# Kernel tuning notes

Hardware: AMD Instinct MI355X
Metric: run time of the kernel (lower is better)

Reference implementation:

```python
import jax, jax.numpy as jnp
import numpy as np

N_STATE = 1024
N_HEAD = 16
HEAD_DIM = N_STATE // N_HEAD


def setup_inputs() -> dict:
    key = jax.random.key(0)
    ks = jax.random.split(key, 8)
    s = 0.02
    return {
        "x": jax.random.normal(ks[0], (4, 1500, N_STATE), dtype=jnp.float32),
        "Wq": jax.random.normal(ks[1], (N_STATE, N_STATE), dtype=jnp.float32) * s,
        "bq": jnp.zeros((N_STATE,), dtype=jnp.float32),
        "Wk": jax.random.normal(ks[2], (N_STATE, N_STATE), dtype=jnp.float32) * s,
        "Wv": jax.random.normal(ks[3], (N_STATE, N_STATE), dtype=jnp.float32) * s,
        "bv": jnp.zeros((N_STATE,), dtype=jnp.float32),
        "Wo": jax.random.normal(ks[4], (N_STATE, N_STATE), dtype=jnp.float32) * s,
        "bo": jnp.zeros((N_STATE,), dtype=jnp.float32),
    }


def reference(x, Wq, bq, Wk, Wv, bv, Wo, bo):
    B, S, _ = x.shape
    scale = HEAD_DIM ** (-0.5)
    # projections (torch Linear: y = x @ W.T + b)
    q = x @ Wq.T + bq
    k = x @ Wk.T
    v = x @ Wv.T + bv
    # [B, H, S, D]
    q = q.reshape(B, S, N_HEAD, HEAD_DIM).transpose(0, 2, 1, 3)
    k = k.reshape(B, S, N_HEAD, HEAD_DIM).transpose(0, 2, 1, 3)
    v = v.reshape(B, S, N_HEAD, HEAD_DIM).transpose(0, 2, 1, 3)
    # scores scaled AFTER the matmul, as in the original (qk * qk_scale)
    qk = jnp.einsum("bhqd,bhkd->bhqk", q, k) * scale
    w = jax.nn.softmax(qk, axis=-1)
    wv = jnp.einsum("bhqk,bhkd->bhqd", w, v)
    wv = wv.transpose(0, 2, 1, 3).reshape(B, S, N_STATE)
    return wv @ Wo.T + bo
```

## Files before the change

kernel.cpp:

```cpp
#include <hip/hip_runtime.h>
#include <stdint.h>

#define S_LEN  1500
#define S_PAD  1536
#define BATCH  4
#define NSTATE 1024
#define NHEAD  16
#define HDIM   64
#define MROWS  6000
#define C1 0.180336879f

typedef __attribute__((ext_vector_type(8)))  short short8;
typedef __attribute__((ext_vector_type(4)))  float floatx4;
typedef __attribute__((ext_vector_type(16))) float floatx16;

__device__ __forceinline__ unsigned short f2bf(float f) {
  union { float f; unsigned int u; } v; v.f = f;
  unsigned int r = v.u + 0x7fffu + ((v.u >> 16) & 1u);
  return (unsigned short)(r >> 16);
}

__device__ __forceinline__ void gld_lds16(const void* g, void* l) {
  __builtin_amdgcn_global_load_lds(
      (const __attribute__((address_space(1))) void*)g,
      (__attribute__((address_space(3))) void*)l, 16, 0, 0);
}

__global__ __launch_bounds__(256) void cvt_all(
    const float* __restrict__ x,  const float* __restrict__ Wq,
    const float* __restrict__ Wk, const float* __restrict__ Wv,
    const float* __restrict__ Wo, unsigned short* __restrict__ dst,
    unsigned short* __restrict__ vt)
{
  const size_t NX   = (size_t)MROWS * NSTATE;
  const size_t NTOT = NX + 4u * 1024u * 1024u;
  size_t e = ((size_t)blockIdx.x * 256 + threadIdx.x) * 4;
  if (e >= NTOT) {
    size_t p = (e - NTOT) >> 2;
    int row = (int)(p / 9);
    int off = (int)(p % 9) * 4;
    uint2 z; z.x = 0u; z.y = 0u;
    *(uint2*)&vt[(size_t)row * S_PAD + 1500 + off] = z;
    return;
  }
  const float* src; size_t off;
  if (e < NX) { src = x; off = e; }
  else {
    size_t t = e - NX;
    int wsel = (int)(t >> 20);
    off = t & ((1u << 20) - 1);
    src = (wsel == 0) ? Wq : (wsel == 1) ? Wk : (wsel == 2) ? Wv : Wo;
  }
  float4 v = *(const float4*)(src + off);
  uint2 o;
  o.x = (unsigned int)f2bf(v.x) | ((unsigned int)f2bf(v.y) << 16);
  o.y = (unsigned int)f2bf(v.z) | ((unsigned int)f2bf(v.w) << 16);
  *(uint2*)(dst + e) = o;
}

__device__ __forceinline__ void gemm128_32(
    const unsigned short* __restrict__ X,
    const unsigned short* __restrict__ W,
    const float* __restrict__ bias,
    void* __restrict__ Yv,
    int m0, int n0, float oscale, int outmode)
{
  __shared__ unsigned short As[2][128 * 32];
  __shared__ unsigned short Bs[2][128 * 32];

  const int tid  = threadIdx.x;
  const int lane = tid & 63;
  const int wid  = tid >> 6;
  const int wm   = (wid & 1) * 64;
  const int wn   = (wid >> 1) * 64;
  const int l31  = lane & 31;
  const int lhi  = lane >> 5;
  const int fr   = (l31 >> 1) & 3;

  floatx16 acc[2][2];
#pragma unroll
  for (int i = 0; i < 2; ++i)
#pragma unroll
    for (int j = 0; j < 2; ++j)
      acc[i][j] = (floatx16)(0.f);

  const int srow = tid >> 2;
  const int logc = (lane & 3) ^ ((srow >> 1) & 3);

  const char* xrp[2];
  const char* wrp[2];
#pragma unroll
  for (int r = 0; r < 2; ++r) {
    int arow = m0 + r * 64 + srow;
    if (arow > MROWS - 1) arow = MROWS - 1;
    xrp[r] = (const char*)X + (size_t)arow * NSTATE * 2 + logc * 16;
    int brow = n0 + r * 64 + srow;
    wrp[r] = (const char*)W + (size_t)brow * NSTATE * 2 + logc * 16;
  }

  for (int k0 = 0; k0 < NSTATE; k0 += 64) {
    __syncthreads();
#pragma unroll
    for (int h = 0; h < 2; ++h) {
      int kb = (k0 + h * 32) * 2;
#pragma unroll
      for (int r = 0; r < 2; ++r) {
        gld_lds16(xrp[r] + kb, (char*)As[h] + r * 4096 + wid * 1024);
        gld_lds16(wrp[r] + kb, (char*)Bs[h] + r * 4096 + wid * 1024);
      }
    }
    __syncthreads();

#pragma unroll
    for (int h = 0; h < 2; ++h) {
      short8 af[2][2], bf[2][2];
#pragma unroll
      for (int mt = 0; mt < 2; ++mt)
#pragma unroll
        for (int kc = 0; kc < 2; ++kc) {
          int row  = wm + mt * 32 + l31;
          int phys = (kc * 2 + lhi) ^ fr;
          af[mt][kc] = *(const short8*)(As[h] + row * 32 + phys * 8);
        }
#pragma unroll
      for (int nt = 0; nt < 2; ++nt)
#pragma unroll
        for (int kc = 0; kc < 2; ++kc) {
          int row  = wn + nt * 32 + l31;
          int phys = (kc * 2 + lhi) ^ fr;
          bf[nt][kc] = *(const short8*)(Bs[h] + row * 32 + phys * 8);
        }
#pragma unroll
      for (int mt = 0; mt < 2; ++mt)
#pragma unroll
        for (int nt = 0; nt < 2; ++nt)
#pragma unroll
          for (int kc = 0; kc < 2; ++kc)
            acc[mt][nt] = __builtin_amdgcn_mfma_f32_32x32x16_bf16(
                af[mt][kc], bf[nt][kc], acc[mt][nt], 0, 0, 0);
    }
  }

  if (outmode == 2) {
    unsigned short* vt = (unsigned short*)Yv;
#pragma unroll
    for (int nt = 0; nt < 2; ++nt) {
      int ng = n0 + wn + nt * 32 + l31;
      float bias_v = bias[ng];
      int d  = ng & 63;
      int hh = ng >> 6;
#pragma unroll
      for (int mt = 0; mt < 2; ++mt)
#pragma unroll
        for (int rq = 0; rq < 4; ++rq) {
          int mgq = m0 + wm + mt * 32 + 8 * rq + 4 * lhi;
          if (mgq < MROWS) {
            int bb = mgq / 1500;
            int s0 = mgq - 1500 * bb;
            float v0 = acc[mt][nt][rq * 4 + 0] + bias_v;
            float v1 = acc[mt][nt][rq * 4 + 1] + bias_v;
            float v2 = acc[mt][nt][rq * 4 + 2] + bias_v;
            float v3 = acc[mt][nt][rq * 4 + 3] + bias_v;
            uint2 pk2;
            pk2.x = (unsigned int)f2bf(v0) | ((unsigned int)f2bf(v1) << 16);
            pk2.y = (unsigned int)f2bf(v2) | ((unsigned int)f2bf(v3) << 16);
            *(uint2*)&vt[(((size_t)bb * NHEAD + hh) * HDIM + d) * S_PAD + s0] = pk2;
          }
        }
    }
  } else {
#pragma unroll
    for (int nt = 0; nt < 2; ++nt) {
      int ng = n0 + wn + nt * 32 + l31;
      float bias_v = bias ? bias[ng] : 0.f;
#pragma unroll
      for (int mt = 0; mt < 2; ++mt)
#pragma unroll
        for (int r = 0; r < 16; ++r) {
          int mg = m0 + wm + mt * 32 + (r & 3) + 8 * (r >> 2) + 4 * lhi;
          if (mg < MROWS) {
            float val = (acc[mt][nt][r] + bias_v) * oscale;
            if (outmode == 1) ((float*)Yv)[(size_t)mg * NSTATE + ng] = val;
            else ((unsigned short*)Yv)[(size_t)mg * NSTATE + ng] = f2bf(val);
          }
        }
    }
  }
}

__global__ __launch_bounds__(256) void proj_qkv(
    const unsigned short* __restrict__ X,
    const unsigned short* __restrict__ Wq, const unsigned short* __restrict__ Wk,
    const unsigned short* __restrict__ Wv,
    const float* __restrict__ bq, const float* __restrict__ bv,
    unsigned short* __restrict__ q, unsigned short* __restrict__ k,
    unsigned short* __restrict__ vt)
{
  const int id  = blockIdx.x;
  const int sid = (id & 7) * 141 + (id >> 3);
  const int z   = sid / 376;
  const int rem = sid - z * 376;
  const int m0  = (rem >> 3) * 128;
  const int n0  = (rem & 7) * 128;

  if (z == 0)      gemm128_32(X, Wq, bq, q,  m0, n0, C1,  0);
  else if (z == 1) gemm128_32(X, Wk, (const float*)nullptr, k, m0, n0, 1.0f, 0);
  else             gemm128_32(X, Wv, bv, vt, m0, n0, 1.0f, 2);
}

__global__ __launch_bounds__(256) void proj_o(
    const unsigned short* __restrict__ X, const unsigned short* __restrict__ W,
    const float* __restrict__ bias, float* __restrict__ Y)
{
  const int id  = blockIdx.x;
  const int sid = (id & 7) * 47 + (id >> 3);
  gemm128_32(X, W, bias, Y, (sid >> 3) * 128, (sid & 7) * 128, 1.0f, 1);
}

#define NHALF 24

__global__ __launch_bounds__(256, 4) void attn32t(
    const unsigned short* __restrict__ Q, const unsigned short* __restrict__ K,
    const unsigned short* __restrict__ VT, unsigned short* __restrict__ O)
{
  __shared__ unsigned short SMEM[16384];
  unsigned short* Os = SMEM;

  const int tid  = threadIdx.x;
  const int lane = tid & 63;
  const int w    = tid >> 6;
  const int l31  = lane & 31;
  const int lhi  = lane >> 5;

  const int id  = blockIdx.x;
  const int sid = (id & 7) * 96 + (id >> 3);
  const int qt  = sid % 12;
  const int hb  = sid / 12;
  const int h   = hb & 15;
  const int b   = hb >> 4;

  const size_t base  = ((size_t)b * S_LEN) * NSTATE + h * HDIM;
  const size_t vbase = (((size_t)b * NHEAD + h) * HDIM) * S_PAD;

  const int srow8 = lane >> 3;
  const int sc3   = lane & 7;
  const int swc   = sc3 ^ srow8;

  const char* kq0 = (const char*)K +
      (base + (size_t)(w * 16 + srow8) * NSTATE + (size_t)swc * 8) * 2;
  const char* kq1 = kq0 + (size_t)8 * NSTATE * 2;
  const char* vq0 = (const char*)VT +
      (vbase + (size_t)(w * 16 + srow8) * S_PAD + (size_t)swc * 8) * 2;
  const char* vq1 = vq0 + (size_t)8 * S_PAD * 2;

  short8 qf[4];
  {
    int qrow = qt * 128 + w * 32 + l31;
    if (qrow > S_LEN - 1) qrow = S_LEN - 1;
    const unsigned short* qp = Q + base + (size_t)qrow * NSTATE;
#pragma unroll
    for (int c = 0; c < 4; ++c)
      qf[c] = *(const short8*)(qp + c * 16 + lhi * 8);
  }

  short8 ones8;
#pragma unroll
  for (int i = 0; i < 8; ++i) ones8[i] = (short)0x3F80;

  floatx16 oacc[2];
  oacc[0] = (floatx16)(0.f);
  oacc[1] = (floatx16)(0.f);
  floatx16 lacc = (floatx16)(0.f);

  auto stageN = [&](int u, int bi) {
    char* kb = (char*)SMEM + bi * 8192;
    char* vb = (char*)SMEM + 16384 + bi * 8192;
    size_t ko = (size_t)u * (64 * NSTATE * 2);
    size_t vo = (size_t)u * (64 * 2);
    gld_lds16(kq0 + ko, kb + (w * 2 + 0) * 1024);
    gld_lds16(kq1 + ko, kb + (w * 2 + 1) * 1024);
    gld_lds16(vq0 + vo, vb + (w * 2 + 0) * 1024);
    gld_lds16(vq1 + vo, vb + (w * 2 + 1) * 1024);
  };
  auto stageC = [&](int bi) {
    char* kb = (char*)SMEM + bi * 8192;
    char* vb = (char*)SMEM + 16384 + bi * 8192;
#pragma unroll
    for (int qq = 0; qq < 2; ++qq) {
      int s = 1472 + w * 16 + qq * 8 + srow8;
      if (s > S_LEN - 1) s = S_LEN - 1;
      gld_lds16((const char*)K + (base + (size_t)s * NSTATE + (size_t)swc * 8) * 2,
                kb + (w * 2 + qq) * 1024);
    }
    size_t vo = (size_t)23 * (64 * 2);
    gld_lds16(vq0 + vo, vb + (w * 2 + 0) * 1024);
    gld_lds16(vq1 + vo, vb + (w * 2 + 1) * 1024);
  };

  stageN(0, 0);
  __syncthreads();

  for (int u = 0; u < NHALF; ++u) {
    const int cur = u & 1;
    if (u < NHALF - 2)       stageN(u + 1, cur ^ 1);
    else if (u == NHALF - 2) stageC(cur ^ 1);

    const unsigned short* Ks  = SMEM + cur * 4096;
    const unsigned short* Vts = SMEM + 8192 + cur * 4096;

#pragma unroll
    for (int kvt = 0; kvt < 2; ++kvt) {
      int row = kvt * 32 + l31;
      floatx16 sacc = (floatx16)(0.f);
      __builtin_amdgcn_s_setprio(1);
#pragma unroll
      for (int c = 0; c < 4; ++c) {
        int phys = (c * 2 + lhi) ^ (row & 7);
        short8 ak = *(const short8*)(Ks + row * 64 + phys * 8);
        sacc = __builtin_amdgcn_mfma_f32_32x32x16_bf16(ak, qf[c], sacc, 0, 0, 0);
      }
      __builtin_amdgcn_s_setprio(0);

      if (u == NHALF - 1) {
        if (kvt == 1) {
#pragma unroll
          for (int r = 0; r < 16; ++r) sacc[r] = -3.0e38f;
        } else {
#pragma unroll
          for (int r = 12; r < 16; ++r) sacc[r] = lhi ? -3.0e38f : sacc[r];
        }
      }

      unsigned int pk[8];
#pragma unroll
      for (int i = 0; i < 8; ++i) {
        float plo = exp2f(sacc[2 * i]);
        float phi = exp2f(sacc[2 * i + 1]);
        unsigned int rr;
        asm("v_cvt_pk_bf16_f32 %0, %1, %2" : "=v"(rr) : "v"(plo), "v"(phi));
        pk[i] = rr;
      }

      unsigned int a0 = pk[0], a1 = pk[1], b0 = pk[2], b1 = pk[3];
      asm("v_permlane32_swap_b32 %0, %1" : "+v"(a0), "+v"(b0));
      asm("v_permlane32_swap_b32 %0, %1" : "+v"(a1), "+v"(b1));
      unsigned int c0 = pk[4], c1 = pk[5], d0 = pk[6], d1 = pk[7];
      asm("v_permlane32_swap_b32 %0, %1" : "+v"(c0), "+v"(d0));
      asm("v_permlane32_swap_b32 %0, %1" : "+v"(c1), "+v"(d1));
      int4 f0i, f1i;
      f0i.x = a0; f0i.y = a1; f0i.z = b0; f0i.w = b1;
      f1i.x = c0; f1i.y = c1; f1i.z = d0; f1i.w = d1;
      short8 f0 = *(short8*)&f0i;
      short8 f1 = *(short8*)&f1i;

      __builtin_amdgcn_s_setprio(1);
      lacc = __builtin_amdgcn_mfma_f32_32x32x16_bf16(ones8, f0, lacc, 0, 0, 0);
      lacc = __builtin_amdgcn_mfma_f32_32x32x16_bf16(ones8, f1, lacc, 0, 0, 0);

#pragma unroll
      for (int dt = 0; dt < 2; ++dt) {
        int d = dt * 32 + l31;
        int p0 = ((kvt * 4 + 0) + lhi) ^ (d & 7);
        int p1 = ((kvt * 4 + 2) + lhi) ^ (d & 7);
        short8 av0 = *(const short8*)(Vts + d * 64 + p0 * 8);
        short8 av1 = *(const short8*)(Vts + d * 64 + p1 * 8);
        oacc[dt] = __builtin_amdgcn_mfma_f32_32x32x16_bf16(av0, f0, oacc[dt], 0, 0, 0);
        oacc[dt] = __builtin_amdgcn_mfma_f32_32x32x16_bf16(av1, f1, oacc[dt], 0, 0, 0);
      }
      __builtin_amdgcn_s_setprio(0);
    }

    __syncthreads();
  }

  float inv = 1.f / lacc[0];

  __syncthreads();
#pragma unroll
  for (int dt = 0; dt < 2; ++dt)
#pragma unroll
    for (int g = 0; g < 4; ++g) {
      int d0 = dt * 32 + g * 8 + lhi * 4;
      float v0 = oacc[dt][4 * g + 0] * inv;
      float v1 = oacc[dt][4 * g + 1] * inv;
      float v2 = oacc[dt][4 * g + 2] * inv;
      float v3 = oacc[dt][4 * g + 3] * inv;
      uint2 pk2;
      pk2.x = (unsigned int)f2bf(v0) | ((unsigned int)f2bf(v1) << 16);
      pk2.y = (unsigned int)f2bf(v2) | ((unsigned int)f2bf(v3) << 16);
      *(uint2*)&Os[(w * 32 + l31) * 72 + d0] = pk2;
    }
  __syncthreads();
#pragma unroll
  for (int pass = 0; pass < 4; ++pass) {
    int e = pass * 256 + tid;
    int row = e >> 3, ch = e & 7;
    int s = qt * 128 + row;
    if (s < S_LEN)
      *(uint4*)&O[base + (size_t)s * NSTATE + ch * 8] = *(const uint4*)&Os[row * 72 + ch * 8];
  }
}

extern "C" void kernel_launch(void* const* d_in, const int* in_sizes, int n_in,
                              void* d_out, int out_size, void* d_ws, size_t ws_size,
                              hipStream_t stream) {
  const float* x  = (const float*)d_in[0];
  const float* Wq = (const float*)d_in[1];
  const float* bq = (const float*)d_in[2];
  const float* Wk = (const float*)d_in[3];
  const float* Wv = (const float*)d_in[4];
  const float* bv = (const float*)d_in[5];
  const float* Wo = (const float*)d_in[6];
  const float* bo = (const float*)d_in[7];
  float* out = (float*)d_out;

  const size_t NX  = (size_t)MROWS * NSTATE;
  const size_t NW  = (size_t)NSTATE * NSTATE;

  unsigned short* xb  = (unsigned short*)d_ws;
  unsigned short* Wqb = xb  + NX;
  unsigned short* Wkb = Wqb + NW;
  unsigned short* Wvb = Wkb + NW;
  unsigned short* Wob = Wvb + NW;
  unsigned short* q   = Wob + NW;
  unsigned short* k   = q + NX;
  unsigned short* vt  = k + NX;
  unsigned short* wv  = xb;

  const size_t n4_total = (NX + 4 * NW) / 4;
  const int main_blocks = (int)(n4_total / 256);
  const int pad_blocks  = (BATCH * NHEAD * HDIM * 9) / 256;
  cvt_all<<<dim3(main_blocks + pad_blocks), dim3(256), 0, stream>>>(
      x, Wq, Wk, Wv, Wo, xb, vt);
  proj_qkv<<<dim3(1128), dim3(256), 0, stream>>>(xb, Wqb, Wkb, Wvb, bq, bv, q, k, vt);
  attn32t<<<dim3(768), dim3(256), 0, stream>>>(q, k, vt, wv);
  proj_o<<<dim3(376), dim3(256), 0, stream>>>(wv, Wob, bo, out);
}
```

Before: 240.3 us.

## Double-buffer GEMM K-loop so global-to-LDS loads overlap MFMA compute

The projection GEMM K-loop now uses the two LDS halves as a ping-pong buffer: it prefetches the next 32-wide K slice while computing on the current one, going from one barrier pair per 64-K step to a single barrier per 32-K step. It also raises wave priority around the MFMA block. The intent is to hide global load latency behind matrix math. The trade-off is more loop iterations with less work each, and a reliance on barrier ordering of the async LDS loads for correctness.

```diff
diff --git a/kernel.cpp b/kernel.cpp
--- a/kernel.cpp
+++ b/kernel.cpp
@@ -98,47 +98,50 @@
     wrp[r] = (const char*)W + (size_t)brow * NSTATE * 2 + logc * 16;
   }
 
-  for (int k0 = 0; k0 < NSTATE; k0 += 64) {
+  auto stage = [&](int t, int bi) {
+    const int kb = t * 64;
+    gld_lds16(xrp[0] + kb, (char*)As[bi] + 0 * 4096 + wid * 1024);
+    gld_lds16(xrp[1] + kb, (char*)As[bi] + 1 * 4096 + wid * 1024);
+    gld_lds16(wrp[0] + kb, (char*)Bs[bi] + 0 * 4096 + wid * 1024);
+    gld_lds16(wrp[1] + kb, (char*)Bs[bi] + 1 * 4096 + wid * 1024);
+  };
+
+  stage(0, 0);
+  __syncthreads();
+
+  for (int t = 0; t < 32; ++t) {
+    const int cur = t & 1;
+    if (t < 31) stage(t + 1, cur ^ 1);
+
+    short8 af[2][2], bf[2][2];
+#pragma unroll
+    for (int mt = 0; mt < 2; ++mt)
+#pragma unroll
+      for (int kc = 0; kc < 2; ++kc) {
+        int row  = wm + mt * 32 + l31;
+        int phys = (kc * 2 + lhi) ^ fr;
+        af[mt][kc] = *(const short8*)(As[cur] + row * 32 + phys * 8);
+      }
+#pragma unroll
+    for (int nt = 0; nt < 2; ++nt)
+#pragma unroll
+      for (int kc = 0; kc < 2; ++kc) {
+        int row  = wn + nt * 32 + l31;
+        int phys = (kc * 2 + lhi) ^ fr;
+        bf[nt][kc] = *(const short8*)(Bs[cur] + row * 32 + phys * 8);
+      }
+    __builtin_amdgcn_s_setprio(1);
+#pragma unroll
+    for (int mt = 0; mt < 2; ++mt)
+#pragma unroll
+      for (int nt = 0; nt < 2; ++nt)
+#pragma unroll
+        for (int kc = 0; kc < 2; ++kc)
+          acc[mt][nt] = __builtin_amdgcn_mfma_f32_32x32x16_bf16(
+              af[mt][kc], bf[nt][kc], acc[mt][nt], 0, 0, 0);
+    __builtin_amdgcn_s_setprio(0);
+
     __syncthreads();
-#pragma unroll
-    for (int h = 0; h < 2; ++h) {
-      int kb = (k0 + h * 32) * 2;
-#pragma unroll
-      for (int r = 0; r < 2; ++r) {
-        gld_lds16(xrp[r] + kb, (char*)As[h] + r * 4096 + wid * 1024);
-        gld_lds16(wrp[r] + kb, (char*)Bs[h] + r * 4096 + wid * 1024);
-      }
-    }
-    __syncthreads();
-
-#pragma unroll
-    for (int h = 0; h < 2; ++h) {
-      short8 af[2][2], bf[2][2];
-#pragma unroll
-      for (int mt = 0; mt < 2; ++mt)
-#pragma unroll
-        for (int kc = 0; kc < 2; ++kc) {
-          int row  = wm + mt * 32 + l31;
-          int phys = (kc * 2 + lhi) ^ fr;
-          af[mt][kc] = *(const short8*)(As[h] + row * 32 + phys * 8);
-        }
-#pragma unroll
-      for (int nt = 0; nt < 2; ++nt)
-#pragma unroll
-        for (int kc = 0; kc < 2; ++kc) {
-          int row  = wn + nt * 32 + l31;
-          int phys = (kc * 2 + lhi) ^ fr;
-          bf[nt][kc] = *(const short8*)(Bs[h] + row * 32 + phys * 8);
-        }
-#pragma unroll
-      for (int mt = 0; mt < 2; ++mt)
-#pragma unroll
-        for (int nt = 0; nt < 2; ++nt)
-#pragma unroll
-          for (int kc = 0; kc < 2; ++kc)
-            acc[mt][nt] = __builtin_amdgcn_mfma_f32_32x32x16_bf16(
-                af[mt][kc], bf[nt][kc], acc[mt][nt], 0, 0, 0);
-    }
   }
 
   if (outmode == 2) {
```

Result: slower. 255.4 us (+6.3%).
